# Performance work log

Hardware: AMD Instinct MI355X
Metric: run time of the kernel (lower is better)

Reference implementation:

```python
import jax, jax.numpy as jnp
import numpy as np

EPS = 1e-5
D_MODEL = 64
D_STATE = 16
D_INNER = 128  # expand=2
DT_RANK = 4    # ceil(64/16)


def _inorm(x):
    # InstanceNorm2d (affine=False), NCHW, biased variance, eps=1e-5
    mu = jnp.mean(x, axis=(2, 3), keepdims=True)
    var = jnp.var(x, axis=(2, 3), keepdims=True)
    return (x - mu) * jax.lax.rsqrt(var + EPS)


def _conv2d(x, w, b=None, groups=1):
    y = jax.lax.conv_general_dilated(x, w, (1, 1), 'SAME',
        dimension_numbers=('NCHW', 'OIHW', 'NCHW'), feature_group_count=groups)
    return y if b is None else y + b[None, :, None, None]


def _layernorm(x, w, b):
    mu = jnp.mean(x, axis=-1, keepdims=True)
    var = jnp.var(x, axis=-1, keepdims=True)
    return (x - mu) * jax.lax.rsqrt(var + EPS) * w + b


def _selective_scan(u, delta, A, Bm, Cm, Dp, delta_bias):
    # u, delta: (B,d,L); A: (d,N); Bm,Cm: (B,N,L); Dp: (d,)
    delta = jax.nn.softplus(delta + delta_bias[None, :, None])
    dA = jnp.exp(jnp.einsum('bdl,dn->lbdn', delta, A))        # (L,B,d,N)
    dBu = jnp.einsum('bdl,bnl->lbdn', delta * u, Bm)          # (L,B,d,N)
    Cl = jnp.transpose(Cm, (2, 0, 1))                         # (L,B,N)
    h0 = jnp.zeros((u.shape[0], u.shape[1], A.shape[1]), u.dtype)

    def step(h, inp):
        dA_l, dBu_l, c = inp
        h = dA_l * h + dBu_l
        return h, jnp.einsum('bdn,bn->bd', h, c)

    _, ys = jax.lax.scan(step, h0, (dA, dBu, Cl))             # ys: (L,B,d)
    return jnp.transpose(ys, (1, 2, 0)) + u * Dp[None, :, None]


def _forward(x, dw3_w, dw3_b, dw5_w, dw5_b, dw7_w, dw7_b, fuse_w, fuse_b,
             in_proj_w, conv2d_w, conv2d_b, x_proj_w, dt_proj_w, dt_proj_b,
             A_log, Dp, out_norm_w, out_norm_b, out_proj_w, cf_w, cf_b):
    C = x.shape[1]
    lrelu = lambda t: jax.nn.leaky_relu(t, 0.01)
    # ---- LRGS: multi-scale depthwise convs + fuse + residual (shortcut=Identity) ----
    feats = [lrelu(_inorm(_conv2d(x, w, b, groups=C)))
             for w, b in ((dw3_w, dw3_b), (dw5_w, dw5_b), (dw7_w, dw7_b))]
    xf = _conv2d(jnp.concatenate(feats, axis=1), fuse_w, fuse_b)
    x1 = lrelu(_inorm(xf)) + x
    # ---- MC_Mamba / SS2D ----
    xh = jnp.transpose(x1, (0, 2, 3, 1))           # (B,H,W,C)
    Bn, H, W, _ = xh.shape
    xz = xh @ in_proj_w.T                          # (B,H,W,2*d_inner)
    xm, z = jnp.split(xz, 2, axis=-1)
    xm = jnp.transpose(xm, (0, 3, 1, 2))           # (B,d_inner,H,W)
    xm = jax.nn.silu(_conv2d(xm, conv2d_w, conv2d_b, groups=D_INNER))
    L = H * W
    x_flat = jnp.transpose(xm.reshape(Bn, D_INNER, L), (0, 2, 1))  # (B,L,d)
    xp = x_flat @ x_proj_w.T
    dt, Bm, Cm = jnp.split(xp, [DT_RANK, DT_RANK + D_STATE], axis=-1)
    # NOTE: faithful to source, nn.Linear applies dt_proj_b here AND it is
    # passed again as delta_bias to the scan (bias applied twice).
    dt = jnp.transpose(dt @ dt_proj_w.T + dt_proj_b, (0, 2, 1))    # (B,d,L)
    A = -jnp.exp(A_log)
    y = _selective_scan(jnp.transpose(x_flat, (0, 2, 1)), dt, A,
                        jnp.transpose(Bm, (0, 2, 1)), jnp.transpose(Cm, (0, 2, 1)),
                        Dp, dt_proj_b)
    y = jnp.transpose(y, (0, 2, 1)).reshape(Bn, H, W, D_INNER)
    y = _layernorm(y, out_norm_w, out_norm_b) * jax.nn.silu(z)
    y = y @ out_proj_w.T                           # (B,H,W,d_model)
    y = jnp.transpose(y, (0, 3, 1, 2))
    y = _inorm(_conv2d(y, cf_w, cf_b))
    return x1 + y


def setup_inputs() -> dict:
    key = jax.random.key(0)
    ks = jax.random.split(key, 12)
    B, C, H, W = 8, D_MODEL, 64, 64
    s = 0.05
    return {
        'x': jax.random.normal(ks[0], (B, C, H, W), jnp.float32),
        'dw3_w': jax.random.normal(ks[1], (C, 1, 3, 3), jnp.float32) * s,
        'dw3_b': jnp.zeros((C,), jnp.float32),
        'dw5_w': jax.random.normal(ks[2], (C, 1, 5, 5), jnp.float32) * s,
        'dw5_b': jnp.zeros((C,), jnp.float32),
        'dw7_w': jax.random.normal(ks[3], (C, 1, 7, 7), jnp.float32) * s,
        'dw7_b': jnp.zeros((C,), jnp.float32),
        'fuse_w': jax.random.normal(ks[4], (C, 3 * C, 1, 1), jnp.float32) * s,
        'fuse_b': jnp.zeros((C,), jnp.float32),
        'in_proj_w': jax.random.normal(ks[5], (2 * D_INNER, D_MODEL), jnp.float32) * s,
        'conv2d_w': jax.random.normal(ks[6], (D_INNER, 1, 3, 3), jnp.float32) * s,
        'conv2d_b': jnp.zeros((D_INNER,), jnp.float32),
        'x_proj_w': jax.random.normal(ks[7], (DT_RANK + 2 * D_STATE, D_INNER), jnp.float32) * s,
        'dt_proj_w': jax.random.uniform(ks[8], (D_INNER, DT_RANK), jnp.float32, -0.5, 0.5),
        'dt_proj_b': jnp.exp(jax.random.uniform(ks[9], (D_INNER,), jnp.float32)
                             * (np.log(0.1) - np.log(0.001)) + np.log(0.001)).astype(jnp.float32),
        'A_log': jnp.log(jnp.tile(jnp.arange(1, D_STATE + 1, dtype=jnp.float32), (D_INNER, 1))),
        'Dp': jnp.ones((D_INNER,), jnp.float32),
        'out_norm_w': jnp.ones((D_INNER,), jnp.float32),
        'out_norm_b': jnp.zeros((D_INNER,), jnp.float32),
        'out_proj_w': jax.random.normal(ks[10], (D_MODEL, D_INNER), jnp.float32) * s,
        'cf_w': jax.random.normal(ks[11], (D_MODEL, D_MODEL, 1, 1), jnp.float32) * s,
        'cf_b': jnp.zeros((D_MODEL,), jnp.float32),
    }


def reference(x, dw3_w, dw3_b, dw5_w, dw5_b, dw7_w, dw7_b, fuse_w, fuse_b,
              in_proj_w, conv2d_w, conv2d_b, x_proj_w, dt_proj_w, dt_proj_b,
              A_log, Dp, out_norm_w, out_norm_b, out_proj_w, cf_w, cf_b):
    return _forward(x, dw3_w, dw3_b, dw5_w, dw5_b, dw7_w, dw7_b, fuse_w, fuse_b,
                    in_proj_w, conv2d_w, conv2d_b, x_proj_w, dt_proj_w, dt_proj_b,
                    A_log, Dp, out_norm_w, out_norm_b, out_proj_w, cf_w, cf_b)
```

## Files before the change

### kernel.cpp

```cpp
#include <hip/hip_runtime.h>
#include <math.h>

#define NB 8
#define NC 64
#define NL 4096
#define NDI 128
#define NN 16
#define CHUNK 16
#define NKCH 256

#define OFF_FEATS 0ull
#define OFF_AC    0ull
#define OFF_XF    6291456ull
#define OFF_BMAT  6291456ull
#define OFF_CMAT  6815744ull
#define OFF_X1    8388608ull
#define OFF_XMRAW 10485760ull
#define OFF_BC    10485760ull
#define OFF_G     10485760ull
#define OFF_Z     14680064ull
#define OFF_YC    14680064ull
#define OFF_PART  16777216ull
#define OFF_XMC   18874368ull
#define OFF_DTM   23068672ull
#define OFF_WF    27262976ull
#define OFF_WCOMB (OFF_WF + 58624ull)
#define WS_NEED_FLOATS (OFF_WF + 66816ull)

#define WF_DW3    0
#define WF_DW5    576
#define WF_DW7    2176
#define WF_B3     5312
#define WF_B5     5376
#define WF_B7     5440
#define WF_FUSE   5504
#define WF_FUSEB  17792
#define WF_C2W    17856
#define WF_C2B    19008
#define WF_XPW    19136
#define WF_DTW    23744
#define WF_DTB    24256
#define WF_A      24384
#define WF_DP     26432
#define WF_ONW    26560
#define WF_ONB    26688
#define WF_OPW    26816
#define WF_CFW    35008
#define WF_CFB    39104
#define WF_INPJ   39168

struct Cvt { const float* src; float* dst; int n; int op; };
struct CvtArgs { Cvt d[22]; int ncvt; const float* cfw; const float* opw; float* wcomb; };

__global__ __launch_bounds__(256) void k0_cvt(CvtArgs a){
  if ((int)blockIdx.x < a.ncvt){
    Cvt c = a.d[blockIdx.x];
    for (int i = threadIdx.x; i < c.n; i += 256){
      float v = c.src[i];
      c.dst[i] = c.op ? -expf(v) : v;
    }
  } else {
    int idx = (blockIdx.x - a.ncvt)*256 + threadIdx.x;
    int c = idx >> 7, kk = idx & 127;
    float s = 0.f;
    #pragma unroll
    for (int j=0;j<64;j++) s += a.cfw[c*64+j] * a.opw[j*128+kk];
    a.wcomb[idx] = s;
  }
}

__global__ __launch_bounds__(256, 4) void k1_dw(const float* __restrict__ x, const float* __restrict__ wf,
                                                float* __restrict__ feats, float* __restrict__ part){
  const int quar = blockIdx.x & 3, c = (blockIdx.x >> 2) & 63, b = blockIdx.x >> 8;
  const int tid = threadIdx.x;
  const int r0 = quar*16;
  __shared__ float xs[22*73];
  __shared__ float red[4][6];
  for (int i = tid; i < 22*73; i += 256) xs[i] = 0.f;
  const float* xp = x + ((size_t)b*64 + c)*NL;
  float v[6];
  #pragma unroll
  for (int k=0;k<6;k++){
    int idx = tid + k*256;
    int j = idx >> 6, w = idx & 63;
    int gr = r0 - 3 + j;
    bool ok = (idx < 1408) && (gr >= 0) && (gr < 64);
    v[k] = ok ? xp[gr*64 + w] : 0.f;
  }
  float w3r[9], w5r[25], w7r[49];
  #pragma unroll
  for (int i=0;i<9;i++)  w3r[i] = wf[WF_DW3 + c*9 + i];
  #pragma unroll
  for (int i=0;i<25;i++) w5r[i] = wf[WF_DW5 + c*25 + i];
  #pragma unroll
  for (int i=0;i<49;i++) w7r[i] = wf[WF_DW7 + c*49 + i];
  float b3 = wf[WF_B3+c], b5 = wf[WF_B5+c], b7 = wf[WF_B7+c];
  __syncthreads();
  #pragma unroll
  for (int k=0;k<6;k++){
    int idx = tid + k*256;
    if (idx < 1408){
      int j = idx >> 6, w = idx & 63;
      xs[j*73 + (w+3)] = v[k];
    }
  }
  __syncthreads();
  float s3=0,q3=0,s5=0,q5=0,s7=0,q7=0;
  float* f3 = feats + ((size_t)b*192 + c) * NL + r0*64;
  float* f5 = f3 + (size_t)64*NL;
  float* f7 = f3 + (size_t)128*NL;
  {
    int p = tid*4;
    int lh = p >> 6, w0 = p & 63;
    float a3[4], a5[4], a7[4];
    #pragma unroll
    for (int i=0;i<4;i++){ a3[i]=b3; a5[i]=b5; a7[i]=b7; }
    #pragma unroll
    for (int dy=0; dy<7; dy++){
      float s[10];
      #pragma unroll
      for (int j=0;j<10;j++) s[j] = xs[(lh+dy)*73 + w0 + j];
      #pragma unroll
      for (int dx=0;dx<7;dx++){
        float wv = w7r[dy*7+dx];
        #pragma unroll
        for (int i=0;i<4;i++) a7[i] += s[dx+i]*wv;
      }
      if (dy>=1 && dy<=5){
        #pragma unroll
        for (int dx=0;dx<5;dx++){
          float wv = w5r[(dy-1)*5+dx];
          #pragma unroll
          for (int i=0;i<4;i++) a5[i] += s[dx+1+i]*wv;
        }
      }
      if (dy>=2 && dy<=4){
        #pragma unroll
        for (int dx=0;dx<3;dx++){
          float wv = w3r[(dy-2)*3+dx];
          #pragma unroll
          for (int i=0;i<4;i++) a3[i] += s[dx+2+i]*wv;
        }
      }
    }
    *(float4*)(f3+p) = make_float4(a3[0],a3[1],a3[2],a3[3]);
    *(float4*)(f5+p) = make_float4(a5[0],a5[1],a5[2],a5[3]);
    *(float4*)(f7+p) = make_float4(a7[0],a7[1],a7[2],a7[3]);
    #pragma unroll
    for (int i=0;i<4;i++){
      s3+=a3[i]; q3+=a3[i]*a3[i];
      s5+=a5[i]; q5+=a5[i]*a5[i];
      s7+=a7[i]; q7+=a7[i]*a7[i];
    }
  }
  int wid = tid>>6, lane = tid&63;
  float v6[6]={s3,q3,s5,q5,s7,q7};
  #pragma unroll
  for (int j=0;j<6;j++){
    float t = v6[j];
    #pragma unroll
    for (int o=32;o>0;o>>=1) t += __shfl_down(t,o);
    if (!lane) red[wid][j]=t;
  }
  __syncthreads();
  if (tid < 3){
    float su = red[0][tid*2]+red[1][tid*2]+red[2][tid*2]+red[3][tid*2];
    float sq = red[0][tid*2+1]+red[1][tid*2+1]+red[2][tid*2+1]+red[3][tid*2+1];
    size_t k = (size_t)(b*192 + tid*64 + c)*8 + quar*2;
    part[k]   = su;
    part[k+1] = sq;
  }
}

__global__ __launch_bounds__(256, 3) void k2_fuse(const float* __restrict__ feats, const float* __restrict__ npart,
                                                  const float* __restrict__ wf, float* __restrict__ xf){
  int og = blockIdx.x >> 8, rem = blockIdx.x & 255;
  int b = rem >> 5, pt = rem & 31;
  int jslot = threadIdx.x >> 5, pxslot = threadIdx.x & 31;
  __shared__ float wlds2[192][44];
  __shared__ float xs[32][128];
  __shared__ float msl[192], rsl[192];
  for (int i = threadIdx.x; i < 192; i += 256){
    const float* pp = npart + (size_t)(b*192+i)*8;
    float su = pp[0]+pp[2]+pp[4]+pp[6], sq = pp[1]+pp[3]+pp[5]+pp[7];
    float m = su*(1.f/NL);
    msl[i] = m;
    rsl[i] = rsqrtf(sq*(1.f/NL) - m*m + 1e-5f);
  }
  {
    const float* Wg = wf + WF_FUSE + og*32*192;
    for (int i = threadIdx.x; i < 6144; i += 256){
      int o = i / 192, k = i % 192;
      wlds2[k][o] = Wg[i];
    }
  }
  float acc[4][4];
  #pragma unroll
  for (int j=0;j<4;j++)
    #pragma unroll
    for (int p=0;p<4;p++) acc[j][p]=0.f;
  const float* fbase = feats + (size_t)b*192*NL + pt*128;
  for (int ch = 0; ch < 6; ch++){
    __syncthreads();
    for (int i = threadIdx.x; i < 1024; i += 256){
      int r = i >> 5, c4 = i & 31;
      int k = ch*32 + r;
      float4 f = *(const float4*)(fbase + (size_t)k*NL + c4*4);
      float m = msl[k], rs = rsl[k];
      float v0=(f.x-m)*rs, v1=(f.y-m)*rs, v2=(f.z-m)*rs, v3=(f.w-m)*rs;
      v0 = v0>0.f?v0:0.01f*v0; v1 = v1>0.f?v1:0.01f*v1;
      v2 = v2>0.f?v2:0.01f*v2; v3 = v3>0.f?v3:0.01f*v3;
      ((float4*)&xs[r][0])[c4] = make_float4(v0,v1,v2,v3);
    }
    __syncthreads();
    #pragma unroll 1
    for (int c = 0; c < 32; c++){
      float a[4];
      #pragma unroll
      for (int p=0;p<4;p++) a[p] = xs[c][pxslot + 32*p];
      float4 w4 = *(const float4*)&wlds2[ch*32+c][jslot*4];
      float wv[4] = {w4.x, w4.y, w4.z, w4.w};
      #pragma unroll
      for (int jj=0;jj<4;jj++)
        #pragma unroll
        for (int p=0;p<4;p++) acc[jj][p] += wv[jj]*a[p];
    }
  }
  #pragma unroll
  for (int jj=0;jj<4;jj++){
    int o = og*32 + jslot*4 + jj;
    float bias = wf[WF_FUSEB + o];
    float* dp = xf + (size_t)b*64*NL + (size_t)o*NL + pt*128;
    #pragma unroll
    for (int p=0;p<4;p++) dp[pxslot + 32*p] = acc[jj][p] + bias;
  }
}

__global__ __launch_bounds__(256) void k3_norm(const float* __restrict__ xf, const float* __restrict__ x,
                                               float* __restrict__ x1){
  const int tid = threadIdx.x;
  const size_t base = (size_t)blockIdx.x * NL;
  float loc[16]; float s=0.f, q=0.f;
  #pragma unroll
  for (int i=0;i<16;i++){ float v = xf[base + tid + i*256]; loc[i]=v; s+=v; q+=v*v; }
  __shared__ float red[4][2];
  int wid = tid>>6, lane = tid&63;
  #pragma unroll
  for (int o=32;o>0;o>>=1){ s += __shfl_down(s,o); q += __shfl_down(q,o); }
  if (!lane){ red[wid][0]=s; red[wid][1]=q; }
  __syncthreads();
  s = red[0][0]+red[1][0]+red[2][0]+red[3][0];
  q = red[0][1]+red[1][1]+red[2][1]+red[3][1];
  float m = s*(1.f/NL), va = q*(1.f/NL)-m*m, rs = rsqrtf(va+1e-5f);
  #pragma unroll
  for (int i=0;i<16;i++){
    int idx = tid + i*256;
    float v = (loc[i]-m)*rs;
    v = v>0.f ? v : 0.01f*v;
    x1[base+idx] = v + x[base+idx];
  }
}

__global__ __launch_bounds__(256, 4) void k4_inproj(const float* __restrict__ x1, const float* __restrict__ wf,
                                                    float* __restrict__ xmraw, float* __restrict__ z){
  int og = blockIdx.x >> 8, rem = blockIdx.x & 255;
  int b = rem >> 5, pt = rem & 31;
  int jslot = threadIdx.x >> 5, pxslot = threadIdx.x & 31;
  __shared__ float wlds2[64][76];
  __shared__ float xs[32][128];
  {
    const float* Wg = wf + WF_INPJ + og*64*64;
    for (int i = threadIdx.x; i < 4096; i += 256){
      int o = i >> 6, k = i & 63;
      wlds2[k][o] = Wg[i];
    }
  }
  float acc[8][4];
  #pragma unroll
  for (int j=0;j<8;j++)
    #pragma unroll
    for (int p=0;p<4;p++) acc[j][p]=0.f;
  const float* xbase = x1 + (size_t)b*64*NL + pt*128;
  for (int ch = 0; ch < 2; ch++){
    __syncthreads();
    for (int i = threadIdx.x; i < 1024; i += 256){
      int r = i >> 5, c4 = i & 31;
      ((float4*)&xs[r][0])[c4] = *(const float4*)(xbase + (size_t)(ch*32+r)*NL + c4*4);
    }
    __syncthreads();
    #pragma unroll 1
    for (int c = 0; c < 32; c++){
      float a[4];
      #pragma unroll
      for (int p=0;p<4;p++) a[p] = xs[c][pxslot + 32*p];
      const float4* wp = (const float4*)&wlds2[ch*32+c][jslot*8];
      float4 w0 = wp[0], w1 = wp[1];
      float wv[8] = {w0.x,w0.y,w0.z,w0.w, w1.x,w1.y,w1.z,w1.w};
      #pragma unroll
      for (int jj=0;jj<8;jj++)
        #pragma unroll
        for (int p=0;p<4;p++) acc[jj][p] += wv[jj]*a[p];
    }
  }
  float* dstbase = (og < 2 ? xmraw + (size_t)b*128*NL + (size_t)(og*64)*NL
                           : z     + (size_t)b*128*NL + (size_t)((og-2)*64)*NL) + pt*128;
  #pragma unroll
  for (int jj=0;jj<8;jj++){
    float* dp = dstbase + (size_t)(jslot*8+jj)*NL;
    #pragma unroll
    for (int p=0;p<4;p++) dp[pxslot + 32*p] = acc[jj][p];
  }
}

__global__ __launch_bounds__(256, 4) void k5_dw3(const float* __restrict__ xmraw, const float* __restrict__ wf,
                                                 float* __restrict__ xmc){
  const int half = blockIdx.x & 1;
  const int d = (blockIdx.x >> 1) & 127;
  const int bd = blockIdx.x >> 1;
  const int tid = threadIdx.x;
  const int r0 = half*32;
  __shared__ float xs[34*69];
  for (int i=tid;i<34*69;i+=256) xs[i]=0.f;
  const float* xp = xmraw + (size_t)bd * NL;
  float v[9];
  #pragma unroll
  for (int k=0;k<9;k++){
    int idx = tid + k*256;
    int j = idx >> 6, w = idx & 63;
    int gr = r0 - 1 + j;
    bool ok = (idx < 2176) && (gr >= 0) && (gr < 64);
    v[k] = ok ? xp[gr*64 + w] : 0.f;
  }
  float wr[9];
  #pragma unroll
  for (int i=0;i<9;i++) wr[i] = wf[WF_C2W + d*9 + i];
  float bb = wf[WF_C2B + d];
  __syncthreads();
  #pragma unroll
  for (int k=0;k<9;k++){
    int idx = tid + k*256;
    if (idx < 2176){
      int j = idx >> 6, w = idx & 63;
      xs[j*69 + (w+1)] = v[k];
    }
  }
  __syncthreads();
  float* op = xmc + (size_t)bd * NL + r0*64;
  #pragma unroll
  for (int g=0; g<2; g++){
    int p = g*1024 + tid*4;
    int lh = p>>6, w0 = p&63;
    float a[4];
    #pragma unroll
    for (int i=0;i<4;i++) a[i]=bb;
    #pragma unroll
    for (int dy=0; dy<3; dy++){
      float s[6];
      #pragma unroll
      for (int j=0;j<6;j++) s[j] = xs[(lh+dy)*69 + w0 + j];
      #pragma unroll
      for (int dx=0;dx<3;dx++){
        float wv = wr[dy*3+dx];
        #pragma unroll
        for (int i=0;i<4;i++) a[i] += s[dx+i]*wv;
      }
    }
    float4 o;
    o.x = a[0]/(1.f+__expf(-a[0]));
    o.y = a[1]/(1.f+__expf(-a[1]));
    o.z = a[2]/(1.f+__expf(-a[2]));
    o.w = a[3]/(1.f+__expf(-a[3]));
    *(float4*)(op+p) = o;
  }
}

__global__ __launch_bounds__(256, 3) void k6_xproj(const float* __restrict__ xmc, const float* __restrict__ wf,
                                                   float* __restrict__ Bm, float* __restrict__ Cm,
                                                   float* __restrict__ dtm){
  int b = blockIdx.x >> 5, pt = blockIdx.x & 31;
  int jslot = threadIdx.x >> 6, pxslot = threadIdx.x & 63;
  __shared__ float wlds2[128][52];
  __shared__ float xs[32][128];
  {
    const float* Wg = wf + WF_XPW;
    for (int i = threadIdx.x; i < 4608; i += 256){
      int o = i >> 7, k = i & 127;
      wlds2[k][(o/9)*12 + (o%9)] = Wg[i];
    }
  }
  float acc[9][2];
  #pragma unroll
  for (int j=0;j<9;j++){ acc[j][0]=0.f; acc[j][1]=0.f; }
  const float* ubase = xmc + (size_t)b*128*NL + pt*128;
  for (int ch = 0; ch < 4; ch++){
    __syncthreads();
    for (int i = threadIdx.x; i < 1024; i += 256){
      int r = i >> 5, c4 = i & 31;
      ((float4*)&xs[r][0])[c4] = *(const float4*)(ubase + (size_t)(ch*32+r)*NL + c4*4);
    }
    __syncthreads();
    #pragma unroll 1
    for (int c = 0; c < 32; c++){
      float a0 = xs[c][pxslot];
      float a1 = xs[c][pxslot + 64];
      const float* wr = &wlds2[ch*32+c][jslot*12];
      float4 wa = *(const float4*)wr;
      float4 wb = *(const float4*)(wr+4);
      float w8 = wr[8];
      float wv[9] = {wa.x,wa.y,wa.z,wa.w, wb.x,wb.y,wb.z,wb.w, w8};
      #pragma unroll
      for (int j=0;j<9;j++){
        acc[j][0] += wv[j]*a0;
        acc[j][1] += wv[j]*a1;
      }
    }
  }
  #pragma unroll
  for (int j=0;j<9;j++){
    int o = jslot*9 + j;
    float* dp;
    if (o < 4)       dp = dtm + ((size_t)b*4 + o)*NL;
    else if (o < 20) dp = Bm  + ((size_t)b*16 + (o-4))*NL;
    else             dp = Cm  + ((size_t)b*16 + (o-20))*NL;
    dp[pt*128 + pxslot]      = acc[j][0];
    dp[pt*128 + pxslot + 64] = acc[j][1];
  }
}

__global__ __launch_bounds__(128, 4) void k7_scan1(const float* __restrict__ xmc, const float* __restrict__ Bm,
                                                   const float* __restrict__ dtm, const float* __restrict__ wf,
                                                   float* __restrict__ Ac, float* __restrict__ Bc){
  int k = blockIdx.x & (NKCH-1), b = blockIdx.x >> 8;
  int d = threadIdx.x;
  int l0 = k*CHUNK;
  __shared__ float xs[128*17];
  __shared__ float Bl2[16*20];
  __shared__ float dtl2[16*4];
  float vx[16], vb[2], vd = 0.f;
  #pragma unroll
  for (int j=0;j<16;j++){
    int i = d + 128*j;
    int ch = i >> 4, px = i & 15;
    vx[j] = xmc[((size_t)b*128+ch)*NL + l0 + px];
  }
  #pragma unroll
  for (int j=0;j<2;j++){
    int i = d + 128*j;
    int n = i >> 4, li = i & 15;
    vb[j] = Bm[((size_t)b*16+n)*NL + l0 + li];
  }
  if (d < 64){ int n = d >> 4, li = d & 15; vd = dtm[((size_t)b*4+n)*NL + l0 + li]; }
  #pragma unroll
  for (int j=0;j<16;j++){
    int i = d + 128*j;
    int ch = i >> 4, px = i & 15;
    xs[ch*17+px] = vx[j];
  }
  #pragma unroll
  for (int j=0;j<2;j++){
    int i = d + 128*j;
    int n = i >> 4, li = i & 15;
    Bl2[li*20+n] = vb[j];
  }
  if (d < 64){ int n = d >> 4, li = d & 15; dtl2[li*4+n] = vd; }
  float A[16], P[16], Q[16];
  const float* Af = wf + WF_A + d*16;
  bool fastA = true;
  #pragma unroll
  for (int n=0;n<16;n++){
    A[n]=Af[n]; P[n]=1.f; Q[n]=0.f;
    fastA = fastA && (fabsf(A[n] + (float)(n+1)) < 1e-3f);
  }
  float w0 = wf[WF_DTW+d*4], w1 = wf[WF_DTW+d*4+1], w2 = wf[WF_DTW+d*4+2], w3 = wf[WF_DTW+d*4+3];
  float db2 = 2.f*wf[WF_DTB+d];
  __syncthreads();
  for (int l=0; l<CHUNK; l++){
    float4 dt4 = ((const float4*)dtl2)[l];
    float tt = w0*dt4.x + w1*dt4.y + w2*dt4.z + w3*dt4.w + db2;
    float de = tt > 20.f ? tt : __logf(1.f+__expf(tt));
    float du = de * xs[d*17+l];
    const float4* bp = (const float4*)(Bl2 + l*20);
    float4 b0 = bp[0], b1 = bp[1], b2 = bp[2], b3 = bp[3];
    float bb[16] = {b0.x,b0.y,b0.z,b0.w, b1.x,b1.y,b1.z,b1.w,
                    b2.x,b2.y,b2.z,b2.w, b3.x,b3.y,b3.z,b3.w};
    if (fastA){
      float r = __expf(-de);
      float ap = 1.f;
      #pragma unroll
      for (int n=0;n<16;n++){
        ap *= r;
        P[n] *= ap;
        Q[n] = ap*Q[n] + du*bb[n];
      }
    } else {
      #pragma unroll
      for (int n=0;n<16;n++){
        float a = __expf(de*A[n]);
        P[n] *= a;
        Q[n] = a*Q[n] + du*bb[n];
      }
    }
  }
  size_t base = (((size_t)k*NB + b)*128 + d)*16;
  #pragma unroll
  for (int i=0;i<4;i++){
    ((float4*)(Ac+base))[i] = make_float4(P[i*4],P[i*4+1],P[i*4+2],P[i*4+3]);
    ((float4*)(Bc+base))[i] = make_float4(Q[i*4],Q[i*4+1],Q[i*4+2],Q[i*4+3]);
  }
}

__global__ __launch_bounds__(128, 2) void k8_mid(const float* Ac, const float* __restrict__ Bc,
                                                 float* Hi){
  int idx = blockIdx.x*128 + threadIdx.x;
  float h = 0.f;
  for (int k0=0;k0<NKCH;k0+=16){
    float av[16], bv[16];
    #pragma unroll
    for (int j=0;j<16;j++){
      size_t o = (size_t)(k0+j)*16384 + idx;
      av[j]=Ac[o]; bv[j]=Bc[o];
    }
    #pragma unroll
    for (int j=0;j<16;j++){
      size_t o = (size_t)(k0+j)*16384 + idx;
      Hi[o] = h;
      h = av[j]*h + bv[j];
    }
  }
}

__global__ __launch_bounds__(128, 4) void k9_scan2(const float* __restrict__ xmc, const float* __restrict__ Bm,
                                                   const float* __restrict__ Cm, const float* __restrict__ dtm,
                                                   const float* __restrict__ z, const float* __restrict__ wf,
                                                   const float* __restrict__ Hi, float* __restrict__ G){
  int k = blockIdx.x & (NKCH-1), b = blockIdx.x >> 8;
  int d = threadIdx.x;
  int l0 = k*CHUNK;
  __shared__ float xs[128*17];
  __shared__ float Bl2[16*20], Cl2[16*20];
  __shared__ float dtl2[16*4];
  __shared__ float red[8][16][2];
  __shared__ float mstat[16], rstat[16];
  float vx[16], vb[2], vc[2], vd = 0.f;
  #pragma unroll
  for (int j=0;j<16;j++){
    int i = d + 128*j;
    int ch = i >> 4, px = i & 15;
    vx[j] = xmc[((size_t)b*128+ch)*NL + l0 + px];
  }
  #pragma unroll
  for (int j=0;j<2;j++){
    int i = d + 128*j;
    int n = i >> 4, li = i & 15;
    vb[j] = Bm[((size_t)b*16+n)*NL + l0 + li];
    vc[j] = Cm[((size_t)b*16+n)*NL + l0 + li];
  }
  if (d < 64){ int n = d >> 4, li = d & 15; vd = dtm[((size_t)b*4+n)*NL + l0 + li]; }
  float A[16], h[16];
  const float* Af = wf + WF_A + d*16;
  size_t hb = (((size_t)k*NB + b)*128 + d)*16;
  bool fastA = true;
  #pragma unroll
  for (int n=0;n<16;n++){
    A[n]=Af[n]; h[n]=Hi[hb+n];
    fastA = fastA && (fabsf(A[n] + (float)(n+1)) < 1e-3f);
  }
  #pragma unroll
  for (int j=0;j<16;j++){
    int i = d + 128*j;
    int ch = i >> 4, px = i & 15;
    xs[ch*17+px] = vx[j];
  }
  #pragma unroll
  for (int j=0;j<2;j++){
    int i = d + 128*j;
    int n = i >> 4, li = i & 15;
    Bl2[li*20+n] = vb[j];
    Cl2[li*20+n] = vc[j];
  }
  if (d < 64){ int n = d >> 4, li = d & 15; dtl2[li*4+n] = vd; }
  float Dv = wf[WF_DP + d];
  float w0 = wf[WF_DTW+d*4], w1 = wf[WF_DTW+d*4+1], w2 = wf[WF_DTW+d*4+2], w3 = wf[WF_DTW+d*4+3];
  float db2 = 2.f*wf[WF_DTB+d];
  __syncthreads();
  for (int l=0; l<CHUNK; l++){
    float4 dt4 = ((const float4*)dtl2)[l];
    float tt = w0*dt4.x + w1*dt4.y + w2*dt4.z + w3*dt4.w + db2;
    float de = tt > 20.f ? tt : __logf(1.f+__expf(tt));
    float uu = xs[d*17+l];
    float du = de * uu;
    float yv = uu * Dv;
    const float4* bp = (const float4*)(Bl2 + l*20);
    const float4* cp = (const float4*)(Cl2 + l*20);
    float4 b0 = bp[0], b1 = bp[1], b2 = bp[2], b3 = bp[3];
    float4 c0 = cp[0], c1 = cp[1], c2 = cp[2], c3 = cp[3];
    float bb[16] = {b0.x,b0.y,b0.z,b0.w, b1.x,b1.y,b1.z,b1.w,
                    b2.x,b2.y,b2.z,b2.w, b3.x,b3.y,b3.z,b3.w};
    float cc[16] = {c0.x,c0.y,c0.z,c0.w, c1.x,c1.y,c1.z,c1.w,
                    c2.x,c2.y,c2.z,c2.w, c3.x,c3.y,c3.z,c3.w};
    if (fastA){
      float r = __expf(-de);
      float ap = 1.f;
      #pragma unroll
      for (int n=0;n<16;n++){
        ap *= r;
        h[n] = ap*h[n] + du*bb[n];
        yv  += h[n]*cc[n];
      }
    } else {
      #pragma unroll
      for (int n=0;n<16;n++){
        float a = __expf(de*A[n]);
        h[n] = a*h[n] + du*bb[n];
        yv  += h[n]*cc[n];
      }
    }
    xs[d*17+l] = yv;
  }
  __syncthreads();
  {
    int px = d & 15, q = d >> 4;
    float s=0.f, qq=0.f;
    #pragma unroll
    for (int j=0;j<16;j++){ float v = xs[(q*16+j)*17+px]; s+=v; qq+=v*v; }
    red[q][px][0]=s; red[q][px][1]=qq;
  }
  __syncthreads();
  if (d < 16){
    float ss=0.f, sq=0.f;
    #pragma unroll
    for (int q=0;q<8;q++){ ss += red[q][d][0]; sq += red[q][d][1]; }
    float m = ss*(1.f/128.f);
    mstat[d] = m;
    rstat[d] = rsqrtf(sq*(1.f/128.f) - m*m + 1e-5f);
  }
  __syncthreads();
  float ow = wf[WF_ONW+d], ob = wf[WF_ONB+d];
  const float* zp = z + ((size_t)b*128+d)*NL + l0;
  float* gp = G + ((size_t)b*128+d)*NL + l0;
  #pragma unroll
  for (int l4=0; l4<CHUNK/4; l4++){
    float4 zv4 = ((const float4*)zp)[l4];
    float zv[4] = {zv4.x, zv4.y, zv4.z, zv4.w};
    float out[4];
    #pragma unroll
    for (int j=0;j<4;j++){
      int l = l4*4+j;
      float t = (xs[d*17+l]-mstat[l])*rstat[l]*ow + ob;
      out[j] = t * (zv[j]/(1.f+__expf(-zv[j])));
    }
    ((float4*)gp)[l4] = make_float4(out[0],out[1],out[2],out[3]);
  }
}

__global__ __launch_bounds__(256, 4) void k11A_proj(const float* __restrict__ G, const float* __restrict__ wf,
                                                    const float* __restrict__ wcomb,
                                                    float* __restrict__ yc, float* __restrict__ part){
  int og = blockIdx.x >> 8, rem = blockIdx.x & 255;
  int b = rem >> 5, pt = rem & 31;
  int jslot = threadIdx.x >> 5, pxslot = threadIdx.x & 31;
  __shared__ float wlds2[128][44];
  __shared__ float xs[32][128];
  {
    const float* Wg = wcomb + og*32*128;
    for (int i = threadIdx.x; i < 4096; i += 256){
      int o = i >> 7, k = i & 127;
      wlds2[k][o] = Wg[i];
    }
  }
  float acc[4][4];
  #pragma unroll
  for (int j=0;j<4;j++)
    #pragma unroll
    for (int p=0;p<4;p++) acc[j][p]=0.f;
  const float* gbase = G + (size_t)b*128*NL + pt*128;
  for (int ch = 0; ch < 4; ch++){
    __syncthreads();
    for (int i = threadIdx.x; i < 1024; i += 256){
      int r = i >> 5, c4 = i & 31;
      ((float4*)&xs[r][0])[c4] = *(const float4*)(gbase + (size_t)(ch*32+r)*NL + c4*4);
    }
    __syncthreads();
    #pragma unroll 1
    for (int c = 0; c < 32; c++){
      float a[4];
      #pragma unroll
      for (int p=0;p<4;p++) a[p] = xs[c][pxslot + 32*p];
      float4 w4 = *(const float4*)&wlds2[ch*32+c][jslot*4];
      float wv[4] = {w4.x, w4.y, w4.z, w4.w};
      #pragma unroll
      for (int jj=0;jj<4;jj++)
        #pragma unroll
        for (int p=0;p<4;p++) acc[jj][p] += wv[jj]*a[p];
    }
  }
  #pragma unroll
  for (int jj=0;jj<4;jj++){
    int cc = og*32 + jslot*4 + jj;
    float bias = wf[WF_CFB + cc];
    float* dp = yc + (size_t)b*64*NL + (size_t)cc*NL + pt*128;
    float sv = 0.f, qv = 0.f;
    #pragma unroll
    for (int p=0;p<4;p++){
      float t = acc[jj][p] + bias;
      dp[pxslot + 32*p] = t;
      sv += t; qv += t*t;
    }
    #pragma unroll
    for (int o=16;o>0;o>>=1){ sv += __shfl_xor(sv,o); qv += __shfl_xor(qv,o); }
    if (pxslot == 0){
      size_t pidx = (((size_t)b*64 + cc)*32 + pt)*2;
      part[pidx] = sv; part[pidx+1] = qv;
    }
  }
}

__global__ __launch_bounds__(256) void k11c_final(const float* __restrict__ yc, const float* __restrict__ part,
                                                  const float* __restrict__ x1, float* __restrict__ out){
  int bc = blockIdx.x;
  __shared__ float sm, sr;
  if (threadIdx.x == 0){
    float s=0.f, q=0.f;
    #pragma unroll
    for (int t2=0;t2<32;t2++){ s += part[((size_t)bc*32+t2)*2]; q += part[((size_t)bc*32+t2)*2+1]; }
    float m = s*(1.f/NL);
    sm = m; sr = rsqrtf(q*(1.f/NL) - m*m + 1e-5f);
  }
  __syncthreads();
  float m = sm, rs = sr;
  size_t base = (size_t)bc*NL;
  for (int i=threadIdx.x;i<NL;i+=256){
    float v = (yc[base+i]-m)*rs;
    out[base+i] = x1[base+i] + v;
  }
}

extern "C" void kernel_launch(void* const* d_in, const int* in_sizes, int n_in,
                              void* d_out, int out_size, void* d_ws, size_t ws_size,
                              hipStream_t stream) {
  if (ws_size < WS_NEED_FLOATS * sizeof(float)) return;
  const float* x     = (const float*)d_in[0];
  const float* dw3w  = (const float*)d_in[1];
  const float* dw3b  = (const float*)d_in[2];
  const float* dw5w  = (const float*)d_in[3];
  const float* dw5b  = (const float*)d_in[4];
  const float* dw7w  = (const float*)d_in[5];
  const float* dw7b  = (const float*)d_in[6];
  const float* fusew = (const float*)d_in[7];
  const float* fuseb = (const float*)d_in[8];
  const float* inpjw = (const float*)d_in[9];
  const float* c2w   = (const float*)d_in[10];
  const float* c2b   = (const float*)d_in[11];
  const float* xpw   = (const float*)d_in[12];
  const float* dtw   = (const float*)d_in[13];
  const float* dtb   = (const float*)d_in[14];
  const float* alog  = (const float*)d_in[15];
  const float* dpv   = (const float*)d_in[16];
  const float* onw   = (const float*)d_in[17];
  const float* onb   = (const float*)d_in[18];
  const float* opw   = (const float*)d_in[19];
  const float* cfw   = (const float*)d_in[20];
  const float* cfb   = (const float*)d_in[21];

  float* ws    = (float*)d_ws;
  float* wf    = ws + OFF_WF;
  float* wcomb = ws + OFF_WCOMB;
  float* feats = ws + OFF_FEATS;
  float* xf    = ws + OFF_XF;
  float* x1    = ws + OFF_X1;
  float* xmraw = ws + OFF_XMRAW;
  float* z     = ws + OFF_Z;
  float* xmc   = ws + OFF_XMC;
  float* Bmw   = ws + OFF_BMAT;
  float* Cmw   = ws + OFF_CMAT;
  float* dtm   = ws + OFF_DTM;
  float* Acb   = ws + OFF_AC;
  float* Bcb   = ws + OFF_BC;
  float* G     = ws + OFF_G;
  float* yc    = ws + OFF_YC;
  float* part  = ws + OFF_PART;

  CvtArgs ca; int ns = 0;
  auto add = [&](const float* s, int off, int n, int op){
    ca.d[ns].src = s; ca.d[ns].dst = wf + off; ca.d[ns].n = n; ca.d[ns].op = op; ns++;
  };
  add(dw3w, WF_DW3, 576, 0);   add(dw5w, WF_DW5, 1600, 0);  add(dw7w, WF_DW7, 3136, 0);
  add(dw3b, WF_B3, 64, 0);     add(dw5b, WF_B5, 64, 0);     add(dw7b, WF_B7, 64, 0);
  add(fusew, WF_FUSE, 12288, 0); add(fuseb, WF_FUSEB, 64, 0);
  add(c2w, WF_C2W, 1152, 0);   add(c2b, WF_C2B, 128, 0);
  add(xpw, WF_XPW, 4608, 0);   add(dtw, WF_DTW, 512, 0);    add(dtb, WF_DTB, 128, 0);
  add(alog, WF_A, 2048, 1);
  add(dpv, WF_DP, 128, 0);
  add(onw, WF_ONW, 128, 0);    add(onb, WF_ONB, 128, 0);
  add(opw, WF_OPW, 8192, 0);
  add(cfw, WF_CFW, 4096, 0);   add(cfb, WF_CFB, 64, 0);
  add(inpjw, WF_INPJ, 16384, 0);
  ca.ncvt = ns; ca.cfw = cfw; ca.opw = opw; ca.wcomb = wcomb;

  k0_cvt<<<ns + 32, 256, 0, stream>>>(ca);
  k1_dw<<<2048, 256, 0, stream>>>(x, wf, feats, part);
  k2_fuse<<<512, 256, 0, stream>>>(feats, part, wf, xf);
  k3_norm<<<512, 256, 0, stream>>>(xf, x, x1);
  k4_inproj<<<1024, 256, 0, stream>>>(x1, wf, xmraw, z);
  k5_dw3<<<2048, 256, 0, stream>>>(xmraw, wf, xmc);
  k6_xproj<<<256, 256, 0, stream>>>(xmc, wf, Bmw, Cmw, dtm);
  k7_scan1<<<2048, 128, 0, stream>>>(xmc, Bmw, dtm, wf, Acb, Bcb);
  k8_mid<<<128, 128, 0, stream>>>(Acb, Bcb, Acb );
  k9_scan2<<<2048, 128, 0, stream>>>(xmc, Bmw, Cmw, dtm, z, wf, Acb , G);
  k11A_proj<<<512, 256, 0, stream>>>(G, wf, wcomb, yc, part);
  k11c_final<<<512, 256, 0, stream>>>(yc, part, x1, (float*)d_out);
}
```

Baseline: 207.1 us.

## Fuse instance-norm stats into fuse conv and drop x1 materialization

The fuse-conv kernel now emits per-tile partial sums and sums of squares of its output. The standalone norm kernel is removed. The in-projection kernel applies the instance norm, leaky ReLU and residual while loading its tile, and the final kernel recomputes x1 from xf and x instead of reading a stored x1. This drops one launch plus a full write and read of x1. In exchange, xf and x are each read twice and the norm arithmetic is done twice.

```diff
diff --git a/kernel.cpp b/kernel.cpp
--- a/kernel.cpp
+++ b/kernel.cpp
@@ -11,10 +11,8 @@
 
 #define OFF_FEATS 0ull
 #define OFF_AC    0ull
-#define OFF_XF    6291456ull
 #define OFF_BMAT  6291456ull
 #define OFF_CMAT  6815744ull
-#define OFF_X1    8388608ull
 #define OFF_XMRAW 10485760ull
 #define OFF_BC    10485760ull
 #define OFF_G     10485760ull
@@ -23,6 +21,8 @@
 #define OFF_PART  16777216ull
 #define OFF_XMC   18874368ull
 #define OFF_DTM   23068672ull
+#define OFF_XF2   23199744ull
+#define OFF_PART2 25296896ull
 #define OFF_WF    27262976ull
 #define OFF_WCOMB (OFF_WF + 58624ull)
 #define WS_NEED_FLOATS (OFF_WF + 66816ull)
@@ -173,7 +173,8 @@
 }
 
 __global__ __launch_bounds__(256, 3) void k2_fuse(const float* __restrict__ feats, const float* __restrict__ npart,
-                                                  const float* __restrict__ wf, float* __restrict__ xf){
+                                                  const float* __restrict__ wf, float* __restrict__ xf,
+                                                  float* __restrict__ part2){
   int og = blockIdx.x >> 8, rem = blockIdx.x & 255;
   int b = rem >> 5, pt = rem & 31;
   int jslot = threadIdx.x >> 5, pxslot = threadIdx.x & 31;
@@ -231,43 +232,40 @@
     int o = og*32 + jslot*4 + jj;
     float bias = wf[WF_FUSEB + o];
     float* dp = xf + (size_t)b*64*NL + (size_t)o*NL + pt*128;
-    #pragma unroll
-    for (int p=0;p<4;p++) dp[pxslot + 32*p] = acc[jj][p] + bias;
-  }
-}
-
-__global__ __launch_bounds__(256) void k3_norm(const float* __restrict__ xf, const float* __restrict__ x,
-                                               float* __restrict__ x1){
-  const int tid = threadIdx.x;
-  const size_t base = (size_t)blockIdx.x * NL;
-  float loc[16]; float s=0.f, q=0.f;
-  #pragma unroll
-  for (int i=0;i<16;i++){ float v = xf[base + tid + i*256]; loc[i]=v; s+=v; q+=v*v; }
-  __shared__ float red[4][2];
-  int wid = tid>>6, lane = tid&63;
-  #pragma unroll
-  for (int o=32;o>0;o>>=1){ s += __shfl_down(s,o); q += __shfl_down(q,o); }
-  if (!lane){ red[wid][0]=s; red[wid][1]=q; }
-  __syncthreads();
-  s = red[0][0]+red[1][0]+red[2][0]+red[3][0];
-  q = red[0][1]+red[1][1]+red[2][1]+red[3][1];
-  float m = s*(1.f/NL), va = q*(1.f/NL)-m*m, rs = rsqrtf(va+1e-5f);
-  #pragma unroll
-  for (int i=0;i<16;i++){
-    int idx = tid + i*256;
-    float v = (loc[i]-m)*rs;
-    v = v>0.f ? v : 0.01f*v;
-    x1[base+idx] = v + x[base+idx];
-  }
-}
-
-__global__ __launch_bounds__(256, 4) void k4_inproj(const float* __restrict__ x1, const float* __restrict__ wf,
+    float sv = 0.f, qv = 0.f;
+    #pragma unroll
+    for (int p=0;p<4;p++){
+      float t = acc[jj][p] + bias;
+      dp[pxslot + 32*p] = t;
+      sv += t; qv += t*t;
+    }
+    #pragma unroll
+    for (int oo=16;oo>0;oo>>=1){ sv += __shfl_xor(sv,oo); qv += __shfl_xor(qv,oo); }
+    if (pxslot == 0){
+      size_t pidx = (((size_t)b*64 + o)*32 + pt)*2;
+      part2[pidx] = sv; part2[pidx+1] = qv;
+    }
+  }
+}
+
+__global__ __launch_bounds__(256, 4) void k4_inproj(const float* __restrict__ xf, const float* __restrict__ x,
+                                                    const float* __restrict__ part2, const float* __restrict__ wf,
                                                     float* __restrict__ xmraw, float* __restrict__ z){
   int og = blockIdx.x >> 8, rem = blockIdx.x & 255;
   int b = rem >> 5, pt = rem & 31;
   int jslot = threadIdx.x >> 5, pxslot = threadIdx.x & 31;
   __shared__ float wlds2[64][76];
   __shared__ float xs[32][128];
+  __shared__ float msl[64], rsl[64];
+  for (int i = threadIdx.x; i < 64; i += 256){
+    const float* pp = part2 + (size_t)(b*64+i)*32*2;
+    float s=0.f, q=0.f;
+    #pragma unroll
+    for (int t2=0;t2<32;t2++){ s += pp[t2*2]; q += pp[t2*2+1]; }
+    float m = s*(1.f/NL);
+    msl[i] = m;
+    rsl[i] = rsqrtf(q*(1.f/NL) - m*m + 1e-5f);
+  }
   {
     const float* Wg = wf + WF_INPJ + og*64*64;
     for (int i = threadIdx.x; i < 4096; i += 256){
@@ -280,12 +278,22 @@
   for (int j=0;j<8;j++)
     #pragma unroll
     for (int p=0;p<4;p++) acc[j][p]=0.f;
-  const float* xbase = x1 + (size_t)b*64*NL + pt*128;
+  const float* fbase = xf + (size_t)b*64*NL + pt*128;
+  const float* xbase = x  + (size_t)b*64*NL + pt*128;
   for (int ch = 0; ch < 2; ch++){
     __syncthreads();
     for (int i = threadIdx.x; i < 1024; i += 256){
       int r = i >> 5, c4 = i & 31;
-      ((float4*)&xs[r][0])[c4] = *(const float4*)(xbase + (size_t)(ch*32+r)*NL + c4*4);
+      int k = ch*32 + r;
+      float4 f  = *(const float4*)(fbase + (size_t)k*NL + c4*4);
+      float4 xv = *(const float4*)(xbase + (size_t)k*NL + c4*4);
+      float m = msl[k], rs = rsl[k];
+      float v0=(f.x-m)*rs, v1=(f.y-m)*rs, v2=(f.z-m)*rs, v3=(f.w-m)*rs;
+      v0 = (v0>0.f?v0:0.01f*v0) + xv.x;
+      v1 = (v1>0.f?v1:0.01f*v1) + xv.y;
+      v2 = (v2>0.f?v2:0.01f*v2) + xv.z;
+      v3 = (v3>0.f?v3:0.01f*v3) + xv.w;
+      ((float4*)&xs[r][0])[c4] = make_float4(v0,v1,v2,v3);
     }
     __syncthreads();
     #pragma unroll 1
@@ -716,22 +724,30 @@
 }
 
 __global__ __launch_bounds__(256) void k11c_final(const float* __restrict__ yc, const float* __restrict__ part,
-                                                  const float* __restrict__ x1, float* __restrict__ out){
+                                                  const float* __restrict__ xf, const float* __restrict__ x,
+                                                  const float* __restrict__ part2, float* __restrict__ out){
   int bc = blockIdx.x;
-  __shared__ float sm, sr;
+  __shared__ float sm, sr, sm2, sr2;
   if (threadIdx.x == 0){
-    float s=0.f, q=0.f;
-    #pragma unroll
-    for (int t2=0;t2<32;t2++){ s += part[((size_t)bc*32+t2)*2]; q += part[((size_t)bc*32+t2)*2+1]; }
+    float s=0.f, q=0.f, s2=0.f, q2=0.f;
+    #pragma unroll
+    for (int t2=0;t2<32;t2++){
+      s  += part [((size_t)bc*32+t2)*2];  q  += part [((size_t)bc*32+t2)*2+1];
+      s2 += part2[((size_t)bc*32+t2)*2];  q2 += part2[((size_t)bc*32+t2)*2+1];
+    }
     float m = s*(1.f/NL);
     sm = m; sr = rsqrtf(q*(1.f/NL) - m*m + 1e-5f);
-  }
-  __syncthreads();
-  float m = sm, rs = sr;
+    float m2 = s2*(1.f/NL);
+    sm2 = m2; sr2 = rsqrtf(q2*(1.f/NL) - m2*m2 + 1e-5f);
+  }
+  __syncthreads();
+  float m = sm, rs = sr, m2 = sm2, rs2 = sr2;
   size_t base = (size_t)bc*NL;
   for (int i=threadIdx.x;i<NL;i+=256){
     float v = (yc[base+i]-m)*rs;
-    out[base+i] = x1[base+i] + v;
+    float t = (xf[base+i]-m2)*rs2;
+    t = t>0.f ? t : 0.01f*t;
+    out[base+i] = t + x[base+i] + v;
   }
 }
 
@@ -766,8 +782,8 @@
   float* wf    = ws + OFF_WF;
   float* wcomb = ws + OFF_WCOMB;
   float* feats = ws + OFF_FEATS;
-  float* xf    = ws + OFF_XF;
-  float* x1    = ws + OFF_X1;
+  float* xf    = ws + OFF_XF2;
+  float* part2 = ws + OFF_PART2;
   float* xmraw = ws + OFF_XMRAW;
   float* z     = ws + OFF_Z;
   float* xmc   = ws + OFF_XMC;
@@ -799,14 +815,13 @@
 
   k0_cvt<<<ns + 32, 256, 0, stream>>>(ca);
   k1_dw<<<2048, 256, 0, stream>>>(x, wf, feats, part);
-  k2_fuse<<<512, 256, 0, stream>>>(feats, part, wf, xf);
-  k3_norm<<<512, 256, 0, stream>>>(xf, x, x1);
-  k4_inproj<<<1024, 256, 0, stream>>>(x1, wf, xmraw, z);
+  k2_fuse<<<512, 256, 0, stream>>>(feats, part, wf, xf, part2);
+  k4_inproj<<<1024, 256, 0, stream>>>(xf, x, part2, wf, xmraw, z);
   k5_dw3<<<2048, 256, 0, stream>>>(xmraw, wf, xmc);
   k6_xproj<<<256, 256, 0, stream>>>(xmc, wf, Bmw, Cmw, dtm);
   k7_scan1<<<2048, 128, 0, stream>>>(xmc, Bmw, dtm, wf, Acb, Bcb);
   k8_mid<<<128, 128, 0, stream>>>(Acb, Bcb, Acb );
   k9_scan2<<<2048, 128, 0, stream>>>(xmc, Bmw, Cmw, dtm, z, wf, Acb , G);
   k11A_proj<<<512, 256, 0, stream>>>(G, wf, wcomb, yc, part);
-  k11c_final<<<512, 256, 0, stream>>>(yc, part, x1, (float*)d_out);
-}
+  k11c_final<<<512, 256, 0, stream>>>(yc, part, xf, x, part2, (float*)d_out);
+}
```

Result: no change. 208.1 us (+0.5%).
